# Kernel tuning notes

Measured on AMD Instinct MI355X. Metric: run time of the kernel, lower is better.

Reference implementation:

```python
import jax, jax.numpy as jnp
import numpy as np

B, L, D, MELS, VOCAB, MAXDUR = 16, 256, 512, 80, 256, 12
T_MAX = L * MAXDUR  # 3072, upper bound on expanded mel length


def setup_inputs() -> dict:
    key = jax.random.key(0)
    ks = jax.random.split(key, 10)
    s = 1.0 / np.sqrt(D)
    return {
        "src": jax.random.randint(ks[0], (B, L), 0, VOCAB),
        "input_dur_inframe": jax.random.randint(ks[1], (B, L), 0, MAXDUR),
        "T": T_MAX,
        "emb_table": jax.random.normal(ks[2], (VOCAB, D), jnp.float32),
        "pos_table": jax.random.normal(ks[3], (L, D), jnp.float32),
        "W_enc": jax.random.normal(ks[4], (D, D), jnp.float32) * s,
        "b_enc": jnp.zeros((D,), jnp.float32),
        "W_dur": jax.random.normal(ks[5], (D, 1), jnp.float32) * s,
        "b_dur": jnp.zeros((1,), jnp.float32),
        "W_dec": jax.random.normal(ks[6], (D, D), jnp.float32) * s,
        "b_dec": jnp.zeros((D,), jnp.float32),
        "W_gen": jax.random.normal(ks[7], (D, MELS), jnp.float32) * s,
        "b_gen": jnp.zeros((MELS,), jnp.float32),
    }


def length_regulate(enc, dur, T):
    """Vectorized equivalent of the nested per-(batch, token) scatter loop.
    Frame f of batch j copies enc[j, k] where k is the token whose duration
    span covers f; frames past the total duration stay zero."""
    csum = jnp.cumsum(dur, axis=-1)                      # [B, L]
    frames = jnp.arange(T)                               # [T]
    # token index per frame: count of tokens with csum <= f
    tok = jax.vmap(lambda c: jnp.searchsorted(c, frames, side="right"))(csum)  # [B, T]
    valid = (tok < dur.shape[1])[..., None]               # [B, T, 1]
    tok = jnp.minimum(tok, dur.shape[1] - 1)
    out = jnp.take_along_axis(enc, tok[..., None], axis=1)  # [B, T, D]
    return out * valid


def reference(src, input_dur_inframe, T, emb_table, pos_table,
              W_enc, b_enc, W_dur, b_dur, W_dec, b_dec, W_gen, b_gen):
    # encode: embedding + positional embedding -> encoder
    x = emb_table[src] + pos_table[None, : src.shape[1], :]        # [B, L, D]
    enc = jax.nn.relu(x @ W_enc + b_enc)                            # [B, L, D]
    # duration predictor on encoder output
    dur_pred = (enc @ W_dur + b_dur)[..., 0]                        # [B, L]
    # length regulator (the custom-kernel hot spot)
    outp = length_regulate(enc, input_dur_inframe, T)               # [B, T, D]
    # decoder + generator, then permute to [B, n_mels, T]
    dec = jax.nn.relu(outp @ W_dec + b_dec)                         # [B, T, D]
    mel = jnp.transpose(dec @ W_gen + b_gen, (0, 2, 1))             # [B, MELS, T]
    return mel, dur_pred
```

## Files before the change

kernel.cpp:

```cpp
#include <hip/hip_runtime.h>

#define D_ 512
#define L_ 256
#define B_ 16
#define T_ 3072
#define MELS_ 80
#define R_ 4096
#define RZ_ 4097
#define CS_ 4104

typedef __bf16 bf16x8 __attribute__((ext_vector_type(8)));
typedef float f32x4 __attribute__((ext_vector_type(4)));

__device__ __forceinline__ unsigned f2bf(float f) {
  union { float f; unsigned u; } x; x.f = f;
  return (x.u + 0x7FFFu + ((x.u >> 16) & 1u)) >> 16;
}
__device__ __forceinline__ float bf2f(unsigned h) {
  union { unsigned u; float f; } x; x.u = h << 16;
  return x.f;
}

__device__ __forceinline__ void transw_dev(const float* __restrict__ src,
                                           unsigned short* __restrict__ dst,
                                           int N, int local, float* sh) {
  int kt = local & 7, nt = local >> 3;
  int k0 = kt * 64, n0 = nt * 64;
  int tid = threadIdx.x;
  int c = tid & 63, r4 = tid >> 6;
  for (int it = 0; it < 16; ++it) {
    int r = it * 4 + r4;
    int n = n0 + c;
    sh[r * 65 + c] = (n < N) ? src[(k0 + r) * N + n] : 0.f;
  }
  __syncthreads();
  for (int it = 0; it < 16; ++it) {
    int r = it * 4 + r4;
    int n = n0 + r;
    if (n < N) dst[n * D_ + k0 + c] = (unsigned short)f2bf(sh[c * 65 + r]);
  }
}

__device__ __forceinline__ void tok_dev(const int* __restrict__ dur,
                                        int* __restrict__ TOK, int b, int* cs) {
  int tid = threadIdx.x;
  cs[tid] = dur[b * L_ + tid];
  for (int off = 1; off < L_; off <<= 1) {
    __syncthreads();
    int v = (tid >= off) ? cs[tid - off] : 0;
    __syncthreads();
    cs[tid] += v;
  }
  __syncthreads();
  for (int t = tid; t < T_; t += 256) {
    int lo = 0, hi = L_;
    while (lo < hi) { int mid = (lo + hi) >> 1; if (cs[mid] <= t) lo = mid + 1; else hi = mid; }
    TOK[b * T_ + t] = (lo < L_) ? (b * L_ + lo) : R_;
  }
}

__global__ void prep_all(const int* __restrict__ src, const int* __restrict__ dur,
                         const float* __restrict__ emb, const float* __restrict__ pos,
                         const float* __restrict__ Wenc, const float* __restrict__ Wdec,
                         const float* __restrict__ Wgen,
                         unsigned short* __restrict__ X, unsigned short* __restrict__ ENC,
                         unsigned short* __restrict__ WET, unsigned short* __restrict__ WDT,
                         unsigned short* __restrict__ WGT, int* __restrict__ TOK) {
  __shared__ float sh[64 * 65];
  int bid = blockIdx.x, tid = threadIdx.x;
  if (bid < 1024) {
    int row = bid * 4 + (tid >> 6);
    int lane = tid & 63;
    int s = src[row];
    int l = row & (L_ - 1);
    int d = lane * 8;
    const float4* ep = (const float4*)(emb + (size_t)s * D_ + d);
    const float4* pp = (const float4*)(pos + (size_t)l * D_ + d);
    float4 a0 = ep[0], a1 = ep[1];
    float4 b0 = pp[0], b1 = pp[1];
    uint4 o;
    o.x = f2bf(a0.x + b0.x) | (f2bf(a0.y + b0.y) << 16);
    o.y = f2bf(a0.z + b0.z) | (f2bf(a0.w + b0.w) << 16);
    o.z = f2bf(a1.x + b1.x) | (f2bf(a1.y + b1.y) << 16);
    o.w = f2bf(a1.z + b1.z) | (f2bf(a1.w + b1.w) << 16);
    *(uint4*)(X + (size_t)row * D_ + d) = o;
  } else if (bid == 1024) {
    if (tid < 64) {
      uint4 z = {0u, 0u, 0u, 0u};
      *(uint4*)(ENC + (size_t)R_ * D_ + tid * 8) = z;
    }
  } else if (bid < 1089) {
    transw_dev(Wenc, WET, 512, bid - 1025, sh);
  } else if (bid < 1153) {
    transw_dev(Wdec, WDT, 512, bid - 1089, sh);
  } else if (bid < 1169) {
    transw_dev(Wgen, WGT, MELS_, bid - 1153, sh);
  } else {
    tok_dev(dur, TOK, bid - 1169, (int*)sh);
  }
}

__global__ __launch_bounds__(256, 4) void gemm64(
    const unsigned short* __restrict__ A, const unsigned short* __restrict__ Bt,
    const float* __restrict__ bias, unsigned short* __restrict__ C,
    int mclamp, int mstore, int ngemm,
    const float* __restrict__ wdur, const float* __restrict__ bdur,
    float* __restrict__ durout) {
  __shared__ short lsA[64 * 64];
  __shared__ short lsB[64 * 64];
  int bid = blockIdx.x, tid = threadIdx.x;
  int lane = tid & 63, w = tid >> 6;

  if (bid >= ngemm) {
    int row = (bid - ngemm) * 4 + w;
    const uint4 e = *(const uint4*)(A + (size_t)row * D_ + lane * 8);
    float4 w0 = *(const float4*)(wdur + lane * 8);
    float4 w1 = *(const float4*)(wdur + lane * 8 + 4);
    float s = 0.f;
    s += bf2f(e.x & 0xffffu) * w0.x;  s += bf2f(e.x >> 16) * w0.y;
    s += bf2f(e.y & 0xffffu) * w0.z;  s += bf2f(e.y >> 16) * w0.w;
    s += bf2f(e.z & 0xffffu) * w1.x;  s += bf2f(e.z >> 16) * w1.y;
    s += bf2f(e.w & 0xffffu) * w1.z;  s += bf2f(e.w >> 16) * w1.w;
    for (int off = 32; off > 0; off >>= 1) s += __shfl_down(s, off, 64);
    if (lane == 0) durout[row] = s + bdur[0];
    return;
  }

  int wm = w >> 1, wn = w & 1;
  int col = lane & 15, quad = lane >> 4;
  int m0 = (bid >> 3) * 64, n0 = (bid & 7) * 64;
  f32x4 acc[2][2] = {};
  for (int ks = 0; ks < 8; ++ks) {
    int k0 = ks * 64;
    __syncthreads();
    for (int it = 0; it < 2; ++it) {
      int linear = it * 256 + tid;
      int row = linear >> 3, p = linear & 7;
      int seg = (p + row) & 7;
      const unsigned short* ga = A + (size_t)min(m0 + row, mclamp) * D_ + k0 + seg * 8;
      const unsigned short* gb = Bt + (size_t)(n0 + row) * D_ + k0 + seg * 8;
      short* la = lsA + (size_t)(it * 256 + (tid & ~63)) * 8;
      short* lb = lsB + (size_t)(it * 256 + (tid & ~63)) * 8;
      __builtin_amdgcn_global_load_lds((const __attribute__((address_space(1))) void*)ga,
                                       (__attribute__((address_space(3))) void*)la, 16, 0, 0);
      __builtin_amdgcn_global_load_lds((const __attribute__((address_space(1))) void*)gb,
                                       (__attribute__((address_space(3))) void*)lb, 16, 0, 0);
    }
    __syncthreads();
    for (int kk = 0; kk < 2; ++kk) {
      int s = kk * 4 + quad;
      bf16x8 af[2], bfr[2];
      for (int mt = 0; mt < 2; ++mt) {
        int r = wm * 32 + mt * 16 + col;
        int p = (s - r) & 7;
        af[mt] = *(const bf16x8*)(lsA + ((size_t)r * 8 + p) * 8);
      }
      for (int nt = 0; nt < 2; ++nt) {
        int r = wn * 32 + nt * 16 + col;
        int p = (s - r) & 7;
        bfr[nt] = *(const bf16x8*)(lsB + ((size_t)r * 8 + p) * 8);
      }
      for (int mt = 0; mt < 2; ++mt)
        for (int nt = 0; nt < 2; ++nt)
          acc[mt][nt] = __builtin_amdgcn_mfma_f32_16x16x32_bf16(af[mt], bfr[nt], acc[mt][nt], 0, 0, 0);
    }
  }
  for (int nt = 0; nt < 2; ++nt) {
    int n = n0 + wn * 32 + nt * 16 + col;
    float bn = bias[n];
    for (int mt = 0; mt < 2; ++mt) {
      int mb = m0 + wm * 32 + mt * 16 + quad * 4;
      for (int i = 0; i < 4; ++i) {
        int m = mb + i;
        if (m < mstore) {
          float v = acc[mt][nt][i] + bn;
          v = v > 0.f ? v : 0.f;
          C[(size_t)m * D_ + n] = (unsigned short)f2bf(v);
        }
      }
    }
  }
}

__global__ void genk(const unsigned short* __restrict__ dec, const unsigned short* __restrict__ wgT,
                     const float* __restrict__ bgen, float* __restrict__ melT) {
  __shared__ float sh[4 * 80 * 16];
  int tid = threadIdx.x;
  int lane = tid & 63, w = tid >> 6;
  int col = lane & 15, quad = lane >> 4;
  int n0 = blockIdx.x * 16;
  int n = n0 + col;
  int nc = min(n, R_);
  f32x4 acc[5] = {};
  const unsigned short* dp = dec + (size_t)nc * D_ + quad * 8;
  for (int ks = 0; ks < 4; ++ks) {
    int k0 = (w * 4 + ks) * 32;
    bf16x8 bfr = *(const bf16x8*)(dp + k0);
    for (int mt = 0; mt < 5; ++mt) {
      bf16x8 afr = *(const bf16x8*)(wgT + (size_t)(mt * 16 + col) * D_ + k0 + quad * 8);
      acc[mt] = __builtin_amdgcn_mfma_f32_16x16x32_bf16(afr, bfr, acc[mt], 0, 0, 0);
    }
  }
  for (int mt = 0; mt < 5; ++mt)
    for (int i = 0; i < 4; ++i) {
      int m = mt * 16 + quad * 4 + i;
      sh[w * 1280 + m * 16 + col] = acc[mt][i];
    }
  __syncthreads();
  for (int j = 0; j < 5; ++j) {
    int idx = j * 256 + tid;
    float v = sh[idx] + sh[1280 + idx] + sh[2560 + idx] + sh[3840 + idx];
    int m = idx >> 4;
    int nn = n0 + (idx & 15);
    if (nn <= R_) melT[(size_t)m * CS_ + nn] = v + bgen[m];
  }
}

__global__ void outk(const int* __restrict__ TOK, const float* __restrict__ melT,
                     float* __restrict__ out) {
  int b = blockIdx.y;
  int tl = blockIdx.x * 128 + (threadIdx.x & 31) * 4;
  int m0 = threadIdx.x >> 5;
  int4 tg = *(const int4*)(TOK + b * T_ + tl);
  float* ob = out + (size_t)b * MELS_ * T_ + tl;
  for (int it = 0; it < 10; ++it) {
    int m = m0 + it * 8;
    const float* mr = melT + (size_t)m * CS_;
    float4 v = make_float4(mr[tg.x], mr[tg.y], mr[tg.z], mr[tg.w]);
    *(float4*)(ob + (size_t)m * T_) = v;
  }
}

extern "C" void kernel_launch(void* const* d_in, const int* in_sizes, int n_in,
                              void* d_out, int out_size, void* d_ws, size_t ws_size,
                              hipStream_t stream) {
  const int* src = (const int*)d_in[0];
  const int* dur = (const int*)d_in[1];
  const float* emb = (const float*)d_in[3];
  const float* pos = (const float*)d_in[4];
  const float* Wenc = (const float*)d_in[5];
  const float* benc = (const float*)d_in[6];
  const float* Wdur = (const float*)d_in[7];
  const float* bdur = (const float*)d_in[8];
  const float* Wdec = (const float*)d_in[9];
  const float* bdec = (const float*)d_in[10];
  const float* Wgen = (const float*)d_in[11];
  const float* bgen = (const float*)d_in[12];

  char* ws = (char*)d_ws;
  unsigned short* X   = (unsigned short*)(ws + 0);
  unsigned short* ENC = (unsigned short*)(ws + 4194304);
  unsigned short* DEC = (unsigned short*)(ws + 8389632);
  unsigned short* WET = (unsigned short*)(ws + 12584960);
  unsigned short* WDT = (unsigned short*)(ws + 13109248);
  unsigned short* WGT = (unsigned short*)(ws + 13633536);
  int* TOK            = (int*)(ws + 13715456);
  float* MELT         = (float*)(ws + 13912064);

  float* out = (float*)d_out;
  float* durout = out + (size_t)B_ * MELS_ * T_;

  prep_all<<<1185, 256, 0, stream>>>(src, dur, emb, pos, Wenc, Wdec, Wgen,
                                     X, ENC, WET, WDT, WGT, TOK);
  gemm64<<<512, 256, 0, stream>>>(X, WET, benc, ENC, R_ - 1, R_, 512,
                                  nullptr, nullptr, nullptr);
  gemm64<<<1544, 256, 0, stream>>>(ENC, WDT, bdec, DEC, R_, RZ_, 520,
                                   Wdur, bdur, durout);
  genk<<<257, 256, 0, stream>>>(DEC, WGT, bgen, MELT);
  outk<<<dim3(24, 16), 256, 0, stream>>>(TOK, MELT, out);
}
```

Baseline: 127.8 us.

## Fuse all stages into one persistent kernel with global grid barriers

Replaces the five kernel launches with a single 512-block kernel. Stages are separated by atomic-counter grid barriers, and a memset resets the counters each call. The duration predictor is folded into the encoder GEMM epilogue through shuffle reductions and atomicAdd into a bias-initialised output. The zero-row decoder output is now computed directly as relu(bdec) instead of being run through an extra GEMM tile. The goal is to remove launch overhead and inter-kernel gaps. In exchange the barriers depend on all 512 blocks being co-resident, the GEMM stages are limited to 512 tiles at 2 blocks per CU, and the atomic float reduction is nondeterministic.

Result: slower. 305.6 us (+139.2%).

```diff
diff --git a/kernel.cpp b/kernel.cpp
--- a/kernel.cpp
+++ b/kernel.cpp
@@ -6,8 +6,8 @@
 #define T_ 3072
 #define MELS_ 80
 #define R_ 4096
-#define RZ_ 4097
 #define CS_ 4104
+#define NBLK 512
 
 typedef __bf16 bf16x8 __attribute__((ext_vector_type(8)));
 typedef float f32x4 __attribute__((ext_vector_type(4)));
@@ -16,9 +16,17 @@
   union { float f; unsigned u; } x; x.f = f;
   return (x.u + 0x7FFFu + ((x.u >> 16) & 1u)) >> 16;
 }
-__device__ __forceinline__ float bf2f(unsigned h) {
-  union { unsigned u; float f; } x; x.u = h << 16;
-  return x.f;
+
+__device__ __forceinline__ void gbar(int* bar, int id) {
+  __syncthreads();
+  if (threadIdx.x == 0) {
+    __threadfence();
+    atomicAdd(&bar[id], 1);
+    while (__hip_atomic_load(&bar[id], __ATOMIC_RELAXED, __HIP_MEMORY_SCOPE_AGENT) < NBLK)
+      __builtin_amdgcn_s_sleep(2);
+    __threadfence();
+  }
+  __syncthreads();
 }
 
 __device__ __forceinline__ void transw_dev(const float* __restrict__ src,
@@ -59,18 +67,98 @@
   }
 }
 
-__global__ void prep_all(const int* __restrict__ src, const int* __restrict__ dur,
-                         const float* __restrict__ emb, const float* __restrict__ pos,
-                         const float* __restrict__ Wenc, const float* __restrict__ Wdec,
-                         const float* __restrict__ Wgen,
-                         unsigned short* __restrict__ X, unsigned short* __restrict__ ENC,
-                         unsigned short* __restrict__ WET, unsigned short* __restrict__ WDT,
-                         unsigned short* __restrict__ WGT, int* __restrict__ TOK) {
-  __shared__ float sh[64 * 65];
+__device__ __forceinline__ void gemm_tile(
+    const unsigned short* __restrict__ A, const unsigned short* __restrict__ Bt,
+    const float* __restrict__ bias, unsigned short* __restrict__ C,
+    int m0, int n0, short* lsA, short* lsB,
+    const float* __restrict__ wdur, float* __restrict__ durout) {
+  int tid = threadIdx.x;
+  int lane = tid & 63, w = tid >> 6;
+  int wm = w >> 1, wn = w & 1;
+  int col = lane & 15, quad = lane >> 4;
+  f32x4 acc[2][2] = {};
+  for (int ks = 0; ks < 8; ++ks) {
+    int k0 = ks * 64;
+    __syncthreads();
+    for (int it = 0; it < 2; ++it) {
+      int linear = it * 256 + tid;
+      int row = linear >> 3, p = linear & 7;
+      int seg = (p + row) & 7;
+      const unsigned short* ga = A + (size_t)(m0 + row) * D_ + k0 + seg * 8;
+      const unsigned short* gb = Bt + (size_t)(n0 + row) * D_ + k0 + seg * 8;
+      short* la = lsA + (size_t)(it * 256 + (tid & ~63)) * 8;
+      short* lb = lsB + (size_t)(it * 256 + (tid & ~63)) * 8;
+      __builtin_amdgcn_global_load_lds((const __attribute__((address_space(1))) void*)ga,
+                                       (__attribute__((address_space(3))) void*)la, 16, 0, 0);
+      __builtin_amdgcn_global_load_lds((const __attribute__((address_space(1))) void*)gb,
+                                       (__attribute__((address_space(3))) void*)lb, 16, 0, 0);
+    }
+    __syncthreads();
+    for (int kk = 0; kk < 2; ++kk) {
+      int s = kk * 4 + quad;
+      bf16x8 af[2], bfr[2];
+      for (int mt = 0; mt < 2; ++mt) {
+        int r = wm * 32 + mt * 16 + col;
+        int p = (s - r) & 7;
+        af[mt] = *(const bf16x8*)(lsA + ((size_t)r * 8 + p) * 8);
+      }
+      for (int nt = 0; nt < 2; ++nt) {
+        int r = wn * 32 + nt * 16 + col;
+        int p = (s - r) & 7;
+        bfr[nt] = *(const bf16x8*)(lsB + ((size_t)r * 8 + p) * 8);
+      }
+      for (int mt = 0; mt < 2; ++mt)
+        for (int nt = 0; nt < 2; ++nt)
+          acc[mt][nt] = __builtin_amdgcn_mfma_f32_16x16x32_bf16(af[mt], bfr[nt], acc[mt][nt], 0, 0, 0);
+    }
+  }
+  float dpart[2][4] = {{0.f,0.f,0.f,0.f},{0.f,0.f,0.f,0.f}};
+  for (int nt = 0; nt < 2; ++nt) {
+    int n = n0 + wn * 32 + nt * 16 + col;
+    float bn = bias[n];
+    float wdn = wdur ? wdur[n] : 0.f;
+    for (int mt = 0; mt < 2; ++mt) {
+      int mb = m0 + wm * 32 + mt * 16 + quad * 4;
+      for (int i = 0; i < 4; ++i) {
+        float v = acc[mt][nt][i] + bn;
+        v = v > 0.f ? v : 0.f;
+        C[(size_t)(mb + i) * D_ + n] = (unsigned short)f2bf(v);
+        dpart[mt][i] += v * wdn;
+      }
+    }
+  }
+  if (wdur) {
+    for (int off = 1; off < 16; off <<= 1)
+      for (int mt = 0; mt < 2; ++mt)
+        for (int i = 0; i < 4; ++i)
+          dpart[mt][i] += __shfl_xor(dpart[mt][i], off, 64);
+    if (col == 0)
+      for (int mt = 0; mt < 2; ++mt)
+        for (int i = 0; i < 4; ++i)
+          atomicAdd(&durout[m0 + wm * 32 + mt * 16 + quad * 4 + i], dpart[mt][i]);
+  }
+}
+
+__global__ __launch_bounds__(256, 2) void fused_all(
+    const int* __restrict__ src, const int* __restrict__ dur,
+    const float* __restrict__ emb, const float* __restrict__ pos,
+    const float* __restrict__ Wenc, const float* __restrict__ benc,
+    const float* __restrict__ Wdur, const float* __restrict__ bdur,
+    const float* __restrict__ Wdec, const float* __restrict__ bdec,
+    const float* __restrict__ Wgen, const float* __restrict__ bgen,
+    unsigned short* __restrict__ X, unsigned short* __restrict__ ENC,
+    unsigned short* __restrict__ DEC, unsigned short* __restrict__ WET,
+    unsigned short* __restrict__ WDT, unsigned short* __restrict__ WGT,
+    int* __restrict__ TOK, float* __restrict__ MELT, int* __restrict__ bar,
+    float* __restrict__ out, float* __restrict__ durout) {
+  __shared__ __align__(16) char smem[20480];
+  short* lsA = (short*)smem;
+  short* lsB = (short*)(smem + 8192);
   int bid = blockIdx.x, tid = threadIdx.x;
-  if (bid < 1024) {
-    int row = bid * 4 + (tid >> 6);
-    int lane = tid & 63;
+  int lane = tid & 63;
+
+  for (int u = 0; u < 2; ++u) {
+    int row = bid * 8 + u * 4 + (tid >> 6);
     int s = src[row];
     int l = row & (L_ - 1);
     int d = lane * 8;
@@ -84,150 +172,78 @@
     o.z = f2bf(a1.x + b1.x) | (f2bf(a1.y + b1.y) << 16);
     o.w = f2bf(a1.z + b1.z) | (f2bf(a1.w + b1.w) << 16);
     *(uint4*)(X + (size_t)row * D_ + d) = o;
-  } else if (bid == 1024) {
+  }
+  if (bid < 64)       transw_dev(Wenc, WET, 512, bid, (float*)smem);
+  else if (bid < 128) transw_dev(Wdec, WDT, 512, bid - 64, (float*)smem);
+  else if (bid < 144) transw_dev(Wgen, WGT, MELS_, bid - 128, (float*)smem);
+  else if (bid < 160) tok_dev(dur, TOK, bid - 144, (int*)smem);
+  else if (bid == 160) {
     if (tid < 64) {
-      uint4 z = {0u, 0u, 0u, 0u};
-      *(uint4*)(ENC + (size_t)R_ * D_ + tid * 8) = z;
-    }
-  } else if (bid < 1089) {
-    transw_dev(Wenc, WET, 512, bid - 1025, sh);
-  } else if (bid < 1153) {
-    transw_dev(Wdec, WDT, 512, bid - 1089, sh);
-  } else if (bid < 1169) {
-    transw_dev(Wgen, WGT, MELS_, bid - 1153, sh);
-  } else {
-    tok_dev(dur, TOK, bid - 1169, (int*)sh);
-  }
-}
-
-__global__ __launch_bounds__(256, 4) void gemm64(
-    const unsigned short* __restrict__ A, const unsigned short* __restrict__ Bt,
-    const float* __restrict__ bias, unsigned short* __restrict__ C,
-    int mclamp, int mstore, int ngemm,
-    const float* __restrict__ wdur, const float* __restrict__ bdur,
-    float* __restrict__ durout) {
-  __shared__ short lsA[64 * 64];
-  __shared__ short lsB[64 * 64];
-  int bid = blockIdx.x, tid = threadIdx.x;
-  int lane = tid & 63, w = tid >> 6;
-
-  if (bid >= ngemm) {
-    int row = (bid - ngemm) * 4 + w;
-    const uint4 e = *(const uint4*)(A + (size_t)row * D_ + lane * 8);
-    float4 w0 = *(const float4*)(wdur + lane * 8);
-    float4 w1 = *(const float4*)(wdur + lane * 8 + 4);
-    float s = 0.f;
-    s += bf2f(e.x & 0xffffu) * w0.x;  s += bf2f(e.x >> 16) * w0.y;
-    s += bf2f(e.y & 0xffffu) * w0.z;  s += bf2f(e.y >> 16) * w0.w;
-    s += bf2f(e.z & 0xffffu) * w1.x;  s += bf2f(e.z >> 16) * w1.y;
-    s += bf2f(e.w & 0xffffu) * w1.z;  s += bf2f(e.w >> 16) * w1.w;
-    for (int off = 32; off > 0; off >>= 1) s += __shfl_down(s, off, 64);
-    if (lane == 0) durout[row] = s + bdur[0];
-    return;
-  }
-
-  int wm = w >> 1, wn = w & 1;
-  int col = lane & 15, quad = lane >> 4;
-  int m0 = (bid >> 3) * 64, n0 = (bid & 7) * 64;
-  f32x4 acc[2][2] = {};
-  for (int ks = 0; ks < 8; ++ks) {
-    int k0 = ks * 64;
-    __syncthreads();
-    for (int it = 0; it < 2; ++it) {
-      int linear = it * 256 + tid;
-      int row = linear >> 3, p = linear & 7;
-      int seg = (p + row) & 7;
-      const unsigned short* ga = A + (size_t)min(m0 + row, mclamp) * D_ + k0 + seg * 8;
-      const unsigned short* gb = Bt + (size_t)(n0 + row) * D_ + k0 + seg * 8;
-      short* la = lsA + (size_t)(it * 256 + (tid & ~63)) * 8;
-      short* lb = lsB + (size_t)(it * 256 + (tid & ~63)) * 8;
-      __builtin_amdgcn_global_load_lds((const __attribute__((address_space(1))) void*)ga,
-                                       (__attribute__((address_space(3))) void*)la, 16, 0, 0);
-      __builtin_amdgcn_global_load_lds((const __attribute__((address_space(1))) void*)gb,
-                                       (__attribute__((address_space(3))) void*)lb, 16, 0, 0);
-    }
-    __syncthreads();
-    for (int kk = 0; kk < 2; ++kk) {
-      int s = kk * 4 + quad;
-      bf16x8 af[2], bfr[2];
-      for (int mt = 0; mt < 2; ++mt) {
-        int r = wm * 32 + mt * 16 + col;
-        int p = (s - r) & 7;
-        af[mt] = *(const bf16x8*)(lsA + ((size_t)r * 8 + p) * 8);
-      }
-      for (int nt = 0; nt < 2; ++nt) {
-        int r = wn * 32 + nt * 16 + col;
-        int p = (s - r) & 7;
-        bfr[nt] = *(const bf16x8*)(lsB + ((size_t)r * 8 + p) * 8);
-      }
-      for (int mt = 0; mt < 2; ++mt)
-        for (int nt = 0; nt < 2; ++nt)
-          acc[mt][nt] = __builtin_amdgcn_mfma_f32_16x16x32_bf16(af[mt], bfr[nt], acc[mt][nt], 0, 0, 0);
-    }
-  }
-  for (int nt = 0; nt < 2; ++nt) {
-    int n = n0 + wn * 32 + nt * 16 + col;
-    float bn = bias[n];
-    for (int mt = 0; mt < 2; ++mt) {
-      int mb = m0 + wm * 32 + mt * 16 + quad * 4;
-      for (int i = 0; i < 4; ++i) {
-        int m = mb + i;
-        if (m < mstore) {
-          float v = acc[mt][nt][i] + bn;
-          v = v > 0.f ? v : 0.f;
-          C[(size_t)m * D_ + n] = (unsigned short)f2bf(v);
-        }
-      }
-    }
-  }
-}
-
-__global__ void genk(const unsigned short* __restrict__ dec, const unsigned short* __restrict__ wgT,
-                     const float* __restrict__ bgen, float* __restrict__ melT) {
-  __shared__ float sh[4 * 80 * 16];
-  int tid = threadIdx.x;
-  int lane = tid & 63, w = tid >> 6;
-  int col = lane & 15, quad = lane >> 4;
-  int n0 = blockIdx.x * 16;
-  int n = n0 + col;
-  int nc = min(n, R_);
-  f32x4 acc[5] = {};
-  const unsigned short* dp = dec + (size_t)nc * D_ + quad * 8;
-  for (int ks = 0; ks < 4; ++ks) {
-    int k0 = (w * 4 + ks) * 32;
-    bf16x8 bfr = *(const bf16x8*)(dp + k0);
-    for (int mt = 0; mt < 5; ++mt) {
-      bf16x8 afr = *(const bf16x8*)(wgT + (size_t)(mt * 16 + col) * D_ + k0 + quad * 8);
-      acc[mt] = __builtin_amdgcn_mfma_f32_16x16x32_bf16(afr, bfr, acc[mt], 0, 0, 0);
-    }
-  }
-  for (int mt = 0; mt < 5; ++mt)
-    for (int i = 0; i < 4; ++i) {
-      int m = mt * 16 + quad * 4 + i;
-      sh[w * 1280 + m * 16 + col] = acc[mt][i];
-    }
-  __syncthreads();
-  for (int j = 0; j < 5; ++j) {
-    int idx = j * 256 + tid;
-    float v = sh[idx] + sh[1280 + idx] + sh[2560 + idx] + sh[3840 + idx];
-    int m = idx >> 4;
-    int nn = n0 + (idx & 15);
-    if (nn <= R_) melT[(size_t)m * CS_ + nn] = v + bgen[m];
-  }
-}
-
-__global__ void outk(const int* __restrict__ TOK, const float* __restrict__ melT,
-                     float* __restrict__ out) {
-  int b = blockIdx.y;
-  int tl = blockIdx.x * 128 + (threadIdx.x & 31) * 4;
-  int m0 = threadIdx.x >> 5;
-  int4 tg = *(const int4*)(TOK + b * T_ + tl);
-  float* ob = out + (size_t)b * MELS_ * T_ + tl;
-  for (int it = 0; it < 10; ++it) {
-    int m = m0 + it * 8;
-    const float* mr = melT + (size_t)m * CS_;
-    float4 v = make_float4(mr[tg.x], mr[tg.y], mr[tg.z], mr[tg.w]);
-    *(float4*)(ob + (size_t)m * T_) = v;
+      int d = lane * 8;
+      float4 c0 = *(const float4*)(bdec + d);
+      float4 c1 = *(const float4*)(bdec + d + 4);
+      uint4 o;
+      o.x = f2bf(fmaxf(c0.x, 0.f)) | (f2bf(fmaxf(c0.y, 0.f)) << 16);
+      o.y = f2bf(fmaxf(c0.z, 0.f)) | (f2bf(fmaxf(c0.w, 0.f)) << 16);
+      o.z = f2bf(fmaxf(c1.x, 0.f)) | (f2bf(fmaxf(c1.y, 0.f)) << 16);
+      o.w = f2bf(fmaxf(c1.z, 0.f)) | (f2bf(fmaxf(c1.w, 0.f)) << 16);
+      *(uint4*)(DEC + (size_t)R_ * D_ + d) = o;
+    }
+  } else if (bid == 161) {
+    float bv = bdur[0];
+    for (int i = tid; i < R_; i += 256) durout[i] = bv;
+  }
+  gbar(bar, 0);
+
+  gemm_tile(X, WET, benc, ENC, (bid >> 3) * 64, (bid & 7) * 64, lsA, lsB, Wdur, durout);
+  gbar(bar, 1);
+
+  gemm_tile(ENC, WDT, bdec, DEC, (bid >> 3) * 64, (bid & 7) * 64, lsA, lsB, nullptr, nullptr);
+  gbar(bar, 2);
+
+  if (bid < 257) {
+    float* shg = (float*)smem;
+    int w = tid >> 6;
+    int col = lane & 15, quad = lane >> 4;
+    int n0 = bid * 16;
+    int n = n0 + col;
+    int nc = min(n, R_);
+    f32x4 acc[5] = {};
+    const unsigned short* dp = DEC + (size_t)nc * D_ + quad * 8;
+    for (int ks = 0; ks < 4; ++ks) {
+      int k0 = (w * 4 + ks) * 32;
+      bf16x8 bfr = *(const bf16x8*)(dp + k0);
+      for (int mt = 0; mt < 5; ++mt) {
+        bf16x8 afr = *(const bf16x8*)(WGT + (size_t)(mt * 16 + col) * D_ + k0 + quad * 8);
+        acc[mt] = __builtin_amdgcn_mfma_f32_16x16x32_bf16(afr, bfr, acc[mt], 0, 0, 0);
+      }
+    }
+    for (int mt = 0; mt < 5; ++mt)
+      for (int i = 0; i < 4; ++i)
+        shg[w * 1280 + (mt * 16 + quad * 4 + i) * 16 + col] = acc[mt][i];
+    __syncthreads();
+    for (int j = 0; j < 5; ++j) {
+      int idx = j * 256 + tid;
+      float v = shg[idx] + shg[1280 + idx] + shg[2560 + idx] + shg[3840 + idx];
+      int m = idx >> 4;
+      int nn = n0 + (idx & 15);
+      if (nn <= R_) MELT[(size_t)m * CS_ + nn] = v + bgen[m];
+    }
+  }
+  gbar(bar, 3);
+
+  if (bid < 384) {
+    int b = bid / 24;
+    int tl = (bid % 24) * 128 + (tid & 31) * 4;
+    int m0 = tid >> 5;
+    int4 tg = *(const int4*)(TOK + b * T_ + tl);
+    float* ob = out + (size_t)b * MELS_ * T_ + tl;
+    for (int it = 0; it < 10; ++it) {
+      int m = m0 + it * 8;
+      const float* mr = MELT + (size_t)m * CS_;
+      float4 v = make_float4(mr[tg.x], mr[tg.y], mr[tg.z], mr[tg.w]);
+      *(float4*)(ob + (size_t)m * T_) = v;
+    }
   }
 }
 
@@ -250,22 +266,20 @@
   char* ws = (char*)d_ws;
   unsigned short* X   = (unsigned short*)(ws + 0);
   unsigned short* ENC = (unsigned short*)(ws + 4194304);
-  unsigned short* DEC = (unsigned short*)(ws + 8389632);
-  unsigned short* WET = (unsigned short*)(ws + 12584960);
-  unsigned short* WDT = (unsigned short*)(ws + 13109248);
-  unsigned short* WGT = (unsigned short*)(ws + 13633536);
-  int* TOK            = (int*)(ws + 13715456);
-  float* MELT         = (float*)(ws + 13912064);
+  unsigned short* DEC = (unsigned short*)(ws + 8388608);
+  unsigned short* WET = (unsigned short*)(ws + 12583936);
+  unsigned short* WDT = (unsigned short*)(ws + 13108224);
+  unsigned short* WGT = (unsigned short*)(ws + 13632512);
+  int* TOK            = (int*)(ws + 13714432);
+  float* MELT         = (float*)(ws + 13911040);
+  int* BAR            = (int*)(ws + 15224320);
 
   float* out = (float*)d_out;
   float* durout = out + (size_t)B_ * MELS_ * T_;
 
-  prep_all<<<1185, 256, 0, stream>>>(src, dur, emb, pos, Wenc, Wdec, Wgen,
-                                     X, ENC, WET, WDT, WGT, TOK);
-  gemm64<<<512, 256, 0, stream>>>(X, WET, benc, ENC, R_ - 1, R_, 512,
-                                  nullptr, nullptr, nullptr);
-  gemm64<<<1544, 256, 0, stream>>>(ENC, WDT, bdec, DEC, R_, RZ_, 520,
-                                   Wdur, bdur, durout);
-  genk<<<257, 256, 0, stream>>>(DEC, WGT, bgen, MELT);
-  outk<<<dim3(24, 16), 256, 0, stream>>>(TOK, MELT, out);
-}
+  hipMemsetAsync(BAR, 0, 16, stream);
+  fused_all<<<NBLK, 256, 0, stream>>>(src, dur, emb, pos, Wenc, benc, Wdur, bdur,
+                                      Wdec, bdec, Wgen, bgen,
+                                      X, ENC, DEC, WET, WDT, WGT, TOK, MELT, BAR,
+                                      out, durout);
+}
```

## Fuse embedding gather into encoder GEMM and keep full A tile in LDS

Applied to the files above, without the earlier changes.

The embedding+positional add and bf16 conversion move out of the prep kernel into the encoder GEMM, which builds the whole 64x512 A tile directly in LDS, so the X intermediate is no longer written and re-read. The decoder GEMM also loads its full 64x512 A tile into LDS once up front instead of per k-step. The duration dot product now handles 16 rows per block, which shrinks that grid. The cost is 64KB+ of LDS per block, so launch bounds drop to 2 blocks and occupancy falls. The encoder GEMM also does redundant gather work across its 8 column blocks.

Result: slower. 145.1 us (+13.6%).

```diff
diff --git a/kernel.cpp b/kernel.cpp
--- a/kernel.cpp
+++ b/kernel.cpp
@@ -6,7 +6,6 @@
 #define T_ 3072
 #define MELS_ 80
 #define R_ 4096
-#define RZ_ 4097
 #define CS_ 4104
 
 typedef __bf16 bf16x8 __attribute__((ext_vector_type(8)));
@@ -59,106 +58,169 @@
   }
 }
 
-__global__ void prep_all(const int* __restrict__ src, const int* __restrict__ dur,
-                         const float* __restrict__ emb, const float* __restrict__ pos,
-                         const float* __restrict__ Wenc, const float* __restrict__ Wdec,
-                         const float* __restrict__ Wgen,
-                         unsigned short* __restrict__ X, unsigned short* __restrict__ ENC,
-                         unsigned short* __restrict__ WET, unsigned short* __restrict__ WDT,
-                         unsigned short* __restrict__ WGT, int* __restrict__ TOK) {
+__global__ void prep_lite(const int* __restrict__ dur,
+                          const float* __restrict__ Wenc, const float* __restrict__ Wdec,
+                          const float* __restrict__ Wgen,
+                          unsigned short* __restrict__ ENC,
+                          unsigned short* __restrict__ WET, unsigned short* __restrict__ WDT,
+                          unsigned short* __restrict__ WGT, int* __restrict__ TOK) {
   __shared__ float sh[64 * 65];
   int bid = blockIdx.x, tid = threadIdx.x;
-  if (bid < 1024) {
-    int row = bid * 4 + (tid >> 6);
-    int lane = tid & 63;
-    int s = src[row];
-    int l = row & (L_ - 1);
-    int d = lane * 8;
-    const float4* ep = (const float4*)(emb + (size_t)s * D_ + d);
-    const float4* pp = (const float4*)(pos + (size_t)l * D_ + d);
-    float4 a0 = ep[0], a1 = ep[1];
-    float4 b0 = pp[0], b1 = pp[1];
-    uint4 o;
-    o.x = f2bf(a0.x + b0.x) | (f2bf(a0.y + b0.y) << 16);
-    o.y = f2bf(a0.z + b0.z) | (f2bf(a0.w + b0.w) << 16);
-    o.z = f2bf(a1.x + b1.x) | (f2bf(a1.y + b1.y) << 16);
-    o.w = f2bf(a1.z + b1.z) | (f2bf(a1.w + b1.w) << 16);
-    *(uint4*)(X + (size_t)row * D_ + d) = o;
-  } else if (bid == 1024) {
+  if (bid < 64)       transw_dev(Wenc, WET, 512, bid, sh);
+  else if (bid < 128) transw_dev(Wdec, WDT, 512, bid - 64, sh);
+  else if (bid < 144) transw_dev(Wgen, WGT, MELS_, bid - 128, sh);
+  else if (bid < 160) tok_dev(dur, TOK, bid - 144, (int*)sh);
+  else {
     if (tid < 64) {
       uint4 z = {0u, 0u, 0u, 0u};
-      *(uint4*)(ENC + (size_t)R_ * D_ + tid * 8) = z;
-    }
-  } else if (bid < 1089) {
-    transw_dev(Wenc, WET, 512, bid - 1025, sh);
-  } else if (bid < 1153) {
-    transw_dev(Wdec, WDT, 512, bid - 1089, sh);
-  } else if (bid < 1169) {
-    transw_dev(Wgen, WGT, MELS_, bid - 1153, sh);
-  } else {
-    tok_dev(dur, TOK, bid - 1169, (int*)sh);
-  }
-}
-
-__global__ __launch_bounds__(256, 4) void gemm64(
-    const unsigned short* __restrict__ A, const unsigned short* __restrict__ Bt,
-    const float* __restrict__ bias, unsigned short* __restrict__ C,
-    int mclamp, int mstore, int ngemm,
+      *(uint4*)(ENC + (size_t)R_ * D_ + (tid & 63) * 8) = z;
+    }
+  }
+}
+
+__global__ __launch_bounds__(256, 2) void gemm_enc(
+    const int* __restrict__ src, const float* __restrict__ emb,
+    const float* __restrict__ pos, const unsigned short* __restrict__ WET,
+    const float* __restrict__ benc, unsigned short* __restrict__ ENC) {
+  __shared__ short lsA[64 * 512];
+  __shared__ short lsB[64 * 64];
+  int tid = threadIdx.x;
+  int lane = tid & 63, w = tid >> 6;
+  int wm = w >> 1, wn = w & 1;
+  int col = lane & 15, quad = lane >> 4;
+  int m0 = (blockIdx.x >> 3) * 64, n0 = (blockIdx.x & 7) * 64;
+
+  {
+    int row = tid >> 2, q = tid & 3;
+    int grow = m0 + row;
+    const float* ep = emb + (size_t)src[grow] * D_;
+    const float* pp = pos + (size_t)(grow & (L_ - 1)) * D_;
+    for (int j = 0; j < 16; ++j) {
+      int k = q * 128 + j * 8;
+      float4 a0 = *(const float4*)(ep + k), a1 = *(const float4*)(ep + k + 4);
+      float4 b0 = *(const float4*)(pp + k), b1 = *(const float4*)(pp + k + 4);
+      uint4 o;
+      o.x = f2bf(a0.x + b0.x) | (f2bf(a0.y + b0.y) << 16);
+      o.y = f2bf(a0.z + b0.z) | (f2bf(a0.w + b0.w) << 16);
+      o.z = f2bf(a1.x + b1.x) | (f2bf(a1.y + b1.y) << 16);
+      o.w = f2bf(a1.z + b1.z) | (f2bf(a1.w + b1.w) << 16);
+      int slot = ((k >> 3) + row) & 63;
+      *(uint4*)(lsA + (size_t)row * 512 + slot * 8) = o;
+    }
+  }
+  __syncthreads();
+
+  f32x4 acc[2][2] = {};
+  for (int ks = 0; ks < 8; ++ks) {
+    __syncthreads();
+    for (int it = 0; it < 2; ++it) {
+      int linear = it * 256 + tid;
+      int brow = linear >> 3, p = linear & 7;
+      int seg = (p + brow) & 7;
+      const unsigned short* gb = WET + (size_t)(n0 + brow) * D_ + ks * 64 + seg * 8;
+      short* lb = lsB + (size_t)(it * 256 + (tid & ~63)) * 8;
+      __builtin_amdgcn_global_load_lds((const __attribute__((address_space(1))) void*)gb,
+                                       (__attribute__((address_space(3))) void*)lb, 16, 0, 0);
+    }
+    __syncthreads();
+    for (int kk = 0; kk < 2; ++kk) {
+      int sl = kk * 4 + quad;
+      int sg = ks * 8 + sl;
+      bf16x8 af[2], bfr[2];
+      for (int mt = 0; mt < 2; ++mt) {
+        int r = wm * 32 + mt * 16 + col;
+        af[mt] = *(const bf16x8*)(lsA + (size_t)r * 512 + ((sg + r) & 63) * 8);
+      }
+      for (int nt = 0; nt < 2; ++nt) {
+        int r = wn * 32 + nt * 16 + col;
+        bfr[nt] = *(const bf16x8*)(lsB + (size_t)r * 64 + ((sl - r) & 7) * 8);
+      }
+      for (int mt = 0; mt < 2; ++mt)
+        for (int nt = 0; nt < 2; ++nt)
+          acc[mt][nt] = __builtin_amdgcn_mfma_f32_16x16x32_bf16(af[mt], bfr[nt], acc[mt][nt], 0, 0, 0);
+    }
+  }
+  for (int nt = 0; nt < 2; ++nt) {
+    int n = n0 + wn * 32 + nt * 16 + col;
+    float bn = benc[n];
+    for (int mt = 0; mt < 2; ++mt) {
+      int mb = m0 + wm * 32 + mt * 16 + quad * 4;
+      for (int i = 0; i < 4; ++i) {
+        float v = acc[mt][nt][i] + bn;
+        v = v > 0.f ? v : 0.f;
+        ENC[(size_t)(mb + i) * D_ + n] = (unsigned short)f2bf(v);
+      }
+    }
+  }
+}
+
+__global__ __launch_bounds__(256, 2) void gemm_dec(
+    const unsigned short* __restrict__ ENC, const unsigned short* __restrict__ WDT,
+    const float* __restrict__ bdec, unsigned short* __restrict__ DEC,
     const float* __restrict__ wdur, const float* __restrict__ bdur,
     float* __restrict__ durout) {
-  __shared__ short lsA[64 * 64];
+  __shared__ short lsA[64 * 512];
   __shared__ short lsB[64 * 64];
   int bid = blockIdx.x, tid = threadIdx.x;
   int lane = tid & 63, w = tid >> 6;
 
-  if (bid >= ngemm) {
-    int row = (bid - ngemm) * 4 + w;
-    const uint4 e = *(const uint4*)(A + (size_t)row * D_ + lane * 8);
+  if (bid >= 520) {
+    int b2 = bid - 520;
     float4 w0 = *(const float4*)(wdur + lane * 8);
     float4 w1 = *(const float4*)(wdur + lane * 8 + 4);
-    float s = 0.f;
-    s += bf2f(e.x & 0xffffu) * w0.x;  s += bf2f(e.x >> 16) * w0.y;
-    s += bf2f(e.y & 0xffffu) * w0.z;  s += bf2f(e.y >> 16) * w0.w;
-    s += bf2f(e.z & 0xffffu) * w1.x;  s += bf2f(e.z >> 16) * w1.y;
-    s += bf2f(e.w & 0xffffu) * w1.z;  s += bf2f(e.w >> 16) * w1.w;
-    for (int off = 32; off > 0; off >>= 1) s += __shfl_down(s, off, 64);
-    if (lane == 0) durout[row] = s + bdur[0];
+    float bv = bdur[0];
+    for (int rep = 0; rep < 4; ++rep) {
+      int row = b2 * 16 + w * 4 + rep;
+      const uint4 e = *(const uint4*)(ENC + (size_t)row * D_ + lane * 8);
+      float s = 0.f;
+      s += bf2f(e.x & 0xffffu) * w0.x;  s += bf2f(e.x >> 16) * w0.y;
+      s += bf2f(e.y & 0xffffu) * w0.z;  s += bf2f(e.y >> 16) * w0.w;
+      s += bf2f(e.z & 0xffffu) * w1.x;  s += bf2f(e.z >> 16) * w1.y;
+      s += bf2f(e.w & 0xffffu) * w1.z;  s += bf2f(e.w >> 16) * w1.w;
+      for (int off = 32; off > 0; off >>= 1) s += __shfl_down(s, off, 64);
+      if (lane == 0) durout[row] = s + bv;
+    }
     return;
   }
 
   int wm = w >> 1, wn = w & 1;
   int col = lane & 15, quad = lane >> 4;
   int m0 = (bid >> 3) * 64, n0 = (bid & 7) * 64;
+
+  for (int it = 0; it < 16; ++it) {
+    int linear = it * 256 + tid;
+    int arow = linear >> 6, p = linear & 63;
+    int seg = (p + arow) & 63;
+    const unsigned short* ga = ENC + (size_t)min(m0 + arow, R_) * D_ + seg * 8;
+    short* la = lsA + (size_t)(it * 256 + (tid & ~63)) * 8;
+    __builtin_amdgcn_global_load_lds((const __attribute__((address_space(1))) void*)ga,
+                                     (__attribute__((address_space(3))) void*)la, 16, 0, 0);
+  }
+
   f32x4 acc[2][2] = {};
   for (int ks = 0; ks < 8; ++ks) {
-    int k0 = ks * 64;
-    __syncthreads();
+    if (ks) __syncthreads();
     for (int it = 0; it < 2; ++it) {
       int linear = it * 256 + tid;
-      int row = linear >> 3, p = linear & 7;
-      int seg = (p + row) & 7;
-      const unsigned short* ga = A + (size_t)min(m0 + row, mclamp) * D_ + k0 + seg * 8;
-      const unsigned short* gb = Bt + (size_t)(n0 + row) * D_ + k0 + seg * 8;
-      short* la = lsA + (size_t)(it * 256 + (tid & ~63)) * 8;
+      int brow = linear >> 3, p = linear & 7;
+      int seg = (p + brow) & 7;
+      const unsigned short* gb = WDT + (size_t)(n0 + brow) * D_ + ks * 64 + seg * 8;
       short* lb = lsB + (size_t)(it * 256 + (tid & ~63)) * 8;
-      __builtin_amdgcn_global_load_lds((const __attribute__((address_space(1))) void*)ga,
-                                       (__attribute__((address_space(3))) void*)la, 16, 0, 0);
       __builtin_amdgcn_global_load_lds((const __attribute__((address_space(1))) void*)gb,
                                        (__attribute__((address_space(3))) void*)lb, 16, 0, 0);
     }
     __syncthreads();
     for (int kk = 0; kk < 2; ++kk) {
-      int s = kk * 4 + quad;
+      int sl = kk * 4 + quad;
+      int sg = ks * 8 + sl;
       bf16x8 af[2], bfr[2];
       for (int mt = 0; mt < 2; ++mt) {
         int r = wm * 32 + mt * 16 + col;
-        int p = (s - r) & 7;
-        af[mt] = *(const bf16x8*)(lsA + ((size_t)r * 8 + p) * 8);
+        af[mt] = *(const bf16x8*)(lsA + (size_t)r * 512 + ((sg - r) & 63) * 8);
       }
       for (int nt = 0; nt < 2; ++nt) {
         int r = wn * 32 + nt * 16 + col;
-        int p = (s - r) & 7;
-        bfr[nt] = *(const bf16x8*)(lsB + ((size_t)r * 8 + p) * 8);
+        bfr[nt] = *(const bf16x8*)(lsB + (size_t)r * 64 + ((sl - r) & 7) * 8);
       }
       for (int mt = 0; mt < 2; ++mt)
         for (int nt = 0; nt < 2; ++nt)
@@ -167,15 +229,15 @@
   }
   for (int nt = 0; nt < 2; ++nt) {
     int n = n0 + wn * 32 + nt * 16 + col;
-    float bn = bias[n];
+    float bn = bdec[n];
     for (int mt = 0; mt < 2; ++mt) {
       int mb = m0 + wm * 32 + mt * 16 + quad * 4;
       for (int i = 0; i < 4; ++i) {
         int m = mb + i;
-        if (m < mstore) {
+        if (m < R_ + 1) {
           float v = acc[mt][nt][i] + bn;
           v = v > 0.f ? v : 0.f;
-          C[(size_t)m * D_ + n] = (unsigned short)f2bf(v);
+          DEC[(size_t)m * D_ + n] = (unsigned short)f2bf(v);
         }
       }
     }
@@ -202,10 +264,8 @@
     }
   }
   for (int mt = 0; mt < 5; ++mt)
-    for (int i = 0; i < 4; ++i) {
-      int m = mt * 16 + quad * 4 + i;
-      sh[w * 1280 + m * 16 + col] = acc[mt][i];
-    }
+    for (int i = 0; i < 4; ++i)
+      sh[w * 1280 + (mt * 16 + quad * 4 + i) * 16 + col] = acc[mt][i];
   __syncthreads();
   for (int j = 0; j < 5; ++j) {
     int idx = j * 256 + tid;
@@ -248,24 +308,20 @@
   const float* bgen = (const float*)d_in[12];
 
   char* ws = (char*)d_ws;
-  unsigned short* X   = (unsigned short*)(ws + 0);
-  unsigned short* ENC = (unsigned short*)(ws + 4194304);
-  unsigned short* DEC = (unsigned short*)(ws + 8389632);
-  unsigned short* WET = (unsigned short*)(ws + 12584960);
-  unsigned short* WDT = (unsigned short*)(ws + 13109248);
-  unsigned short* WGT = (unsigned short*)(ws + 13633536);
-  int* TOK            = (int*)(ws + 13715456);
-  float* MELT         = (float*)(ws + 13912064);
+  unsigned short* ENC = (unsigned short*)(ws + 0);
+  unsigned short* DEC = (unsigned short*)(ws + 4195328);
+  unsigned short* WET = (unsigned short*)(ws + 8390656);
+  unsigned short* WDT = (unsigned short*)(ws + 8914944);
+  unsigned short* WGT = (unsigned short*)(ws + 9439232);
+  int* TOK            = (int*)(ws + 9521152);
+  float* MELT         = (float*)(ws + 9717760);
 
   float* out = (float*)d_out;
   float* durout = out + (size_t)B_ * MELS_ * T_;
 
-  prep_all<<<1185, 256, 0, stream>>>(src, dur, emb, pos, Wenc, Wdec, Wgen,
-                                     X, ENC, WET, WDT, WGT, TOK);
-  gemm64<<<512, 256, 0, stream>>>(X, WET, benc, ENC, R_ - 1, R_, 512,
-                                  nullptr, nullptr, nullptr);
-  gemm64<<<1544, 256, 0, stream>>>(ENC, WDT, bdec, DEC, R_, RZ_, 520,
-                                   Wdur, bdur, durout);
+  prep_lite<<<161, 256, 0, stream>>>(dur, Wenc, Wdec, Wgen, ENC, WET, WDT, WGT, TOK);
+  gemm_enc<<<512, 256, 0, stream>>>(src, emb, pos, WET, benc, ENC);
+  gemm_dec<<<776, 256, 0, stream>>>(ENC, WDT, bdec, DEC, Wdur, bdur, durout);
   genk<<<257, 256, 0, stream>>>(DEC, WGT, bgen, MELT);
   outk<<<dim3(24, 16), 256, 0, stream>>>(TOK, MELT, out);
 }
```

## Replace LDS-staged GEMM with direct register loads and batch duration rows

Applied to the files above, without the earlier changes.

The GEMM kernel stops staging A and B tiles through LDS with global_load_lds and barriers. Each wave now loads its bf16x8 MFMA fragments straight from global memory in a fully unrolled K loop, and launch bounds are relaxed to 2 blocks per SM. The duration-predictor tail blocks now handle 16 rows each instead of 4, which cuts that grid from 1544 to 776 blocks. This removes barrier and LDS traffic but gives up shared-tile reuse, so redundant global and L2 reads go up and memory coalescing may be worse.

Result: slower. 149.1 us (+16.7%).

```diff
diff --git a/kernel.cpp b/kernel.cpp
--- a/kernel.cpp
+++ b/kernel.cpp
@@ -6,7 +6,6 @@
 #define T_ 3072
 #define MELS_ 80
 #define R_ 4096
-#define RZ_ 4097
 #define CS_ 4104
 
 typedef __bf16 bf16x8 __attribute__((ext_vector_type(8)));
@@ -87,7 +86,7 @@
   } else if (bid == 1024) {
     if (tid < 64) {
       uint4 z = {0u, 0u, 0u, 0u};
-      *(uint4*)(ENC + (size_t)R_ * D_ + tid * 8) = z;
+      *(uint4*)(ENC + (size_t)R_ * D_ + (tid & 63) * 8) = z;
     }
   } else if (bid < 1089) {
     transw_dev(Wenc, WET, 512, bid - 1025, sh);
@@ -100,71 +99,57 @@
   }
 }
 
-__global__ __launch_bounds__(256, 4) void gemm64(
+__global__ __launch_bounds__(256, 2) void gemm_reg(
     const unsigned short* __restrict__ A, const unsigned short* __restrict__ Bt,
     const float* __restrict__ bias, unsigned short* __restrict__ C,
     int mclamp, int mstore, int ngemm,
     const float* __restrict__ wdur, const float* __restrict__ bdur,
     float* __restrict__ durout) {
-  __shared__ short lsA[64 * 64];
-  __shared__ short lsB[64 * 64];
   int bid = blockIdx.x, tid = threadIdx.x;
   int lane = tid & 63, w = tid >> 6;
 
-  if (bid >= ngemm) {
-    int row = (bid - ngemm) * 4 + w;
-    const uint4 e = *(const uint4*)(A + (size_t)row * D_ + lane * 8);
+  if (durout && bid >= ngemm) {
+    int b2 = bid - ngemm;
     float4 w0 = *(const float4*)(wdur + lane * 8);
     float4 w1 = *(const float4*)(wdur + lane * 8 + 4);
-    float s = 0.f;
-    s += bf2f(e.x & 0xffffu) * w0.x;  s += bf2f(e.x >> 16) * w0.y;
-    s += bf2f(e.y & 0xffffu) * w0.z;  s += bf2f(e.y >> 16) * w0.w;
-    s += bf2f(e.z & 0xffffu) * w1.x;  s += bf2f(e.z >> 16) * w1.y;
-    s += bf2f(e.w & 0xffffu) * w1.z;  s += bf2f(e.w >> 16) * w1.w;
-    for (int off = 32; off > 0; off >>= 1) s += __shfl_down(s, off, 64);
-    if (lane == 0) durout[row] = s + bdur[0];
+    float bv = bdur[0];
+    for (int rep = 0; rep < 4; ++rep) {
+      int row = b2 * 16 + w * 4 + rep;
+      const uint4 e = *(const uint4*)(A + (size_t)row * D_ + lane * 8);
+      float s = 0.f;
+      s += bf2f(e.x & 0xffffu) * w0.x;  s += bf2f(e.x >> 16) * w0.y;
+      s += bf2f(e.y & 0xffffu) * w0.z;  s += bf2f(e.y >> 16) * w0.w;
+      s += bf2f(e.z & 0xffffu) * w1.x;  s += bf2f(e.z >> 16) * w1.y;
+      s += bf2f(e.w & 0xffffu) * w1.z;  s += bf2f(e.w >> 16) * w1.w;
+      for (int off = 32; off > 0; off >>= 1) s += __shfl_down(s, off, 64);
+      if (lane == 0) durout[row] = s + bv;
+    }
     return;
   }
 
   int wm = w >> 1, wn = w & 1;
   int col = lane & 15, quad = lane >> 4;
   int m0 = (bid >> 3) * 64, n0 = (bid & 7) * 64;
+
+  const unsigned short* ap0 = A + (size_t)min(m0 + wm * 32 + col, mclamp) * D_ + quad * 8;
+  const unsigned short* ap1 = A + (size_t)min(m0 + wm * 32 + 16 + col, mclamp) * D_ + quad * 8;
+  const unsigned short* bp0 = Bt + (size_t)(n0 + wn * 32 + col) * D_ + quad * 8;
+  const unsigned short* bp1 = Bt + (size_t)(n0 + wn * 32 + 16 + col) * D_ + quad * 8;
+
   f32x4 acc[2][2] = {};
-  for (int ks = 0; ks < 8; ++ks) {
-    int k0 = ks * 64;
-    __syncthreads();
-    for (int it = 0; it < 2; ++it) {
-      int linear = it * 256 + tid;
-      int row = linear >> 3, p = linear & 7;
-      int seg = (p + row) & 7;
-      const unsigned short* ga = A + (size_t)min(m0 + row, mclamp) * D_ + k0 + seg * 8;
-      const unsigned short* gb = Bt + (size_t)(n0 + row) * D_ + k0 + seg * 8;
-      short* la = lsA + (size_t)(it * 256 + (tid & ~63)) * 8;
-      short* lb = lsB + (size_t)(it * 256 + (tid & ~63)) * 8;
-      __builtin_amdgcn_global_load_lds((const __attribute__((address_space(1))) void*)ga,
-                                       (__attribute__((address_space(3))) void*)la, 16, 0, 0);
-      __builtin_amdgcn_global_load_lds((const __attribute__((address_space(1))) void*)gb,
-                                       (__attribute__((address_space(3))) void*)lb, 16, 0, 0);
-    }
-    __syncthreads();
-    for (int kk = 0; kk < 2; ++kk) {
-      int s = kk * 4 + quad;
-      bf16x8 af[2], bfr[2];
-      for (int mt = 0; mt < 2; ++mt) {
-        int r = wm * 32 + mt * 16 + col;
-        int p = (s - r) & 7;
-        af[mt] = *(const bf16x8*)(lsA + ((size_t)r * 8 + p) * 8);
-      }
-      for (int nt = 0; nt < 2; ++nt) {
-        int r = wn * 32 + nt * 16 + col;
-        int p = (s - r) & 7;
-        bfr[nt] = *(const bf16x8*)(lsB + ((size_t)r * 8 + p) * 8);
-      }
-      for (int mt = 0; mt < 2; ++mt)
-        for (int nt = 0; nt < 2; ++nt)
-          acc[mt][nt] = __builtin_amdgcn_mfma_f32_16x16x32_bf16(af[mt], bfr[nt], acc[mt][nt], 0, 0, 0);
-    }
-  }
+#pragma unroll
+  for (int k2 = 0; k2 < 16; ++k2) {
+    int ko = k2 * 32;
+    bf16x8 a0 = *(const bf16x8*)(ap0 + ko);
+    bf16x8 a1 = *(const bf16x8*)(ap1 + ko);
+    bf16x8 b0 = *(const bf16x8*)(bp0 + ko);
+    bf16x8 b1 = *(const bf16x8*)(bp1 + ko);
+    acc[0][0] = __builtin_amdgcn_mfma_f32_16x16x32_bf16(a0, b0, acc[0][0], 0, 0, 0);
+    acc[0][1] = __builtin_amdgcn_mfma_f32_16x16x32_bf16(a0, b1, acc[0][1], 0, 0, 0);
+    acc[1][0] = __builtin_amdgcn_mfma_f32_16x16x32_bf16(a1, b0, acc[1][0], 0, 0, 0);
+    acc[1][1] = __builtin_amdgcn_mfma_f32_16x16x32_bf16(a1, b1, acc[1][1], 0, 0, 0);
+  }
+
   for (int nt = 0; nt < 2; ++nt) {
     int n = n0 + wn * 32 + nt * 16 + col;
     float bn = bias[n];
@@ -202,10 +187,8 @@
     }
   }
   for (int mt = 0; mt < 5; ++mt)
-    for (int i = 0; i < 4; ++i) {
-      int m = mt * 16 + quad * 4 + i;
-      sh[w * 1280 + m * 16 + col] = acc[mt][i];
-    }
+    for (int i = 0; i < 4; ++i)
+      sh[w * 1280 + (mt * 16 + quad * 4 + i) * 16 + col] = acc[mt][i];
   __syncthreads();
   for (int j = 0; j < 5; ++j) {
     int idx = j * 256 + tid;
@@ -262,10 +245,10 @@
 
   prep_all<<<1185, 256, 0, stream>>>(src, dur, emb, pos, Wenc, Wdec, Wgen,
                                      X, ENC, WET, WDT, WGT, TOK);
-  gemm64<<<512, 256, 0, stream>>>(X, WET, benc, ENC, R_ - 1, R_, 512,
-                                  nullptr, nullptr, nullptr);
-  gemm64<<<1544, 256, 0, stream>>>(ENC, WDT, bdec, DEC, R_, RZ_, 520,
-                                   Wdur, bdur, durout);
+  gemm_reg<<<512, 256, 0, stream>>>(X, WET, benc, ENC, R_ - 1, R_, 512,
+                                    nullptr, nullptr, nullptr);
+  gemm_reg<<<776, 256, 0, stream>>>(ENC, WDT, bdec, DEC, R_, R_ + 1, 520,
+                                    Wdur, bdur, durout);
   genk<<<257, 256, 0, stream>>>(DEC, WGT, bgen, MELT);
   outk<<<dim3(24, 16), 256, 0, stream>>>(TOK, MELT, out);
 }
```
